# Performance work log

Measured on AMD Instinct MI355X. Metric: run time of the kernel, lower is better.

## Reference

```python
import jax, jax.numpy as jnp
import numpy as np

DIM = 384
HEADS = 6
K = 10          # default k of DynamicGraphAttention
HID = 1536      # int(dim * mlp_ratio)
LN_EPS = 1e-5


def layernorm(x, g, b):
    m = jnp.mean(x, -1, keepdims=True)
    var = jnp.mean((x - m) ** 2, -1, keepdims=True)
    return (x - m) * jax.lax.rsqrt(var + LN_EPS) * g + b


def setup_inputs() -> dict:
    key = jax.random.key(0)
    ks = jax.random.split(key, 12)
    B, N, M, C = 16, 1024, 512, DIM
    s = 0.02
    return dict(
        q=jax.random.normal(ks[0], (B, N, C), jnp.float32),
        v=jax.random.normal(ks[1], (B, M, C), jnp.float32),
        q_pos=jax.random.normal(ks[2], (B, N, 3), jnp.float32),
        v_pos=jax.random.normal(ks[3], (B, M, 3), jnp.float32),
        norm1_g=jnp.ones((C,), jnp.float32), norm1_b=jnp.zeros((C,), jnp.float32),
        qkv_w=jax.random.normal(ks[4], (C, 3 * C), jnp.float32) * s,  # qkv_bias=False
        proj_w=jax.random.normal(ks[5], (C, C), jnp.float32) * s,
        proj_b=jnp.zeros((C,), jnp.float32),
        normq_g=jnp.ones((C,), jnp.float32), normq_b=jnp.zeros((C,), jnp.float32),
        normv_g=jnp.ones((C,), jnp.float32), normv_b=jnp.zeros((C,), jnp.float32),
        knn_w=jax.random.normal(ks[6], (2 * C, C), jnp.float32) * s,
        knn_b=jnp.zeros((C,), jnp.float32),
        norm2_g=jnp.ones((C,), jnp.float32), norm2_b=jnp.zeros((C,), jnp.float32),
        fc1_w=jax.random.normal(ks[7], (C, HID), jnp.float32) * s,
        fc1_b=jnp.zeros((HID,), jnp.float32),
        fc2_w=jax.random.normal(ks[8], (HID, C), jnp.float32) * s,
        fc2_b=jnp.zeros((C,), jnp.float32),
    )


def reference(q, v, q_pos, v_pos,
              norm1_g, norm1_b, qkv_w, proj_w, proj_b,
              normq_g, normq_b, normv_g, normv_b, knn_w, knn_b,
              norm2_g, norm2_b, fc1_w, fc1_b, fc2_w, fc2_b):
    B, N, C = q.shape
    D = C // HEADS

    # --- multi-head self-attention with pre-norm residual ---
    x = layernorm(q, norm1_g, norm1_b)
    qkv = (x @ qkv_w).reshape(B, N, 3, HEADS, D)
    qh, kh, vh = qkv[:, :, 0], qkv[:, :, 1], qkv[:, :, 2]   # [B,N,H,D]
    attn = jnp.einsum('bnhd,bmhd->bhnm', qh, kh) * (D ** -0.5)
    attn = jax.nn.softmax(attn, axis=-1)
    sa = jnp.einsum('bhnm,bmhd->bnhd', attn, vh).reshape(B, N, C)
    sa = sa @ proj_w + proj_b
    q = q + sa

    # --- dynamic graph cross-attention (knn gather + diff-concat MLP + max) ---
    nq = layernorm(q, normq_g, normq_b)          # [B,N,C]
    nv = layernorm(v, normv_g, normv_b)          # [B,M,C]
    # squared distances between query and kv positions: [B,N,M]
    d = (jnp.sum(q_pos ** 2, -1)[:, :, None]
         + jnp.sum(v_pos ** 2, -1)[:, None, :]
         - 2.0 * jnp.einsum('bnc,bmc->bnm', q_pos, v_pos))
    _, idx = jax.lax.top_k(-d, K)                # K nearest neighbors, [B,N,K]
    local_v = jax.vmap(lambda vv, ii: vv[ii])(nv, idx)   # [B,N,K,C]
    qe = nq[:, :, None, :]                                # [B,N,1,C]
    feat = jnp.concatenate(
        [local_v - qe, jnp.broadcast_to(qe, local_v.shape)], axis=-1)  # [B,N,K,2C]
    g = jax.nn.leaky_relu(feat @ knn_w + knn_b, negative_slope=0.2)
    q = q + jnp.max(g, axis=-2)                  # max over K neighbors

    # --- MLP with pre-norm residual ---
    h = layernorm(q, norm2_g, norm2_b)
    h = jax.nn.gelu(h @ fc1_w + fc1_b, approximate=False)
    h = h @ fc2_w + fc2_b
    return q + h
```

## Files before the change

### kernel.cpp

```cpp
#include <hip/hip_runtime.h>
#include <hip/hip_bf16.h>

#define CDIM 384
#define NHEAD 6
#define DHEAD 64
#define BB 16
#define NQ 1024
#define MV 512
#define HIDD 1536
#define KNN 10

typedef __attribute__((ext_vector_type(8))) __bf16 bf16x8;
typedef __attribute__((ext_vector_type(4))) float f32x4;
typedef __attribute__((ext_vector_type(4))) short short4v;

__global__ void cast_all_kernel(const float* __restrict__ qkv_w, const float* __restrict__ proj_w,
                                const float* __restrict__ knn_w, const float* __restrict__ fc1_w,
                                const float* __restrict__ fc2_w,
                                __hip_bfloat16* __restrict__ Wqkv_t,
                                __hip_bfloat16* __restrict__ Wproj_t,
                                __hip_bfloat16* __restrict__ W1_t,
                                __hip_bfloat16* __restrict__ Wd_t,
                                __hip_bfloat16* __restrict__ Wfc1_t,
                                __hip_bfloat16* __restrict__ Wfc2_t) {
  __shared__ float t1[32][33];
  __shared__ float t2[32][33];
  int gid = blockIdx.x;
  int tx = threadIdx.x, ty = threadIdx.y;
  if (gid >= 576 && gid < 720) {
    int id = gid - 576;
    int k0 = (id % 12) * 32, n0 = (id / 12) * 32;
#pragma unroll
    for (int i = 0; i < 4; i++) {
      int k = k0 + ty + i * 8;
      float w1 = knn_w[(size_t)k * CDIM + n0 + tx];
      float w2 = knn_w[(size_t)(CDIM + k) * CDIM + n0 + tx];
      t1[ty + i * 8][tx] = w1;
      t2[ty + i * 8][tx] = w2 - w1;
    }
    __syncthreads();
#pragma unroll
    for (int i = 0; i < 4; i++) {
      W1_t[(size_t)(n0 + ty + i * 8) * CDIM + k0 + tx] = __float2bfloat16(t1[tx][ty + i * 8]);
      Wd_t[(size_t)(n0 + ty + i * 8) * CDIM + k0 + tx] = __float2bfloat16(t2[tx][ty + i * 8]);
    }
    return;
  }
  const float* W;
  __hip_bfloat16* Wt;
  int Kd, Nd, k0, n0;
  if (gid < 432) {
    W = qkv_w; Wt = Wqkv_t; Kd = 384; Nd = 1152;
    k0 = (gid % 12) * 32; n0 = (gid / 12) * 32;
  } else if (gid < 576) {
    int id = gid - 432;
    W = proj_w; Wt = Wproj_t; Kd = 384; Nd = 384;
    k0 = (id % 12) * 32; n0 = (id / 12) * 32;
  } else if (gid < 1296) {
    int id = gid - 720;
    W = fc1_w; Wt = Wfc1_t; Kd = 384; Nd = 1536;
    k0 = (id % 12) * 32; n0 = (id / 12) * 32;
  } else {
    int id = gid - 1296;
    W = fc2_w; Wt = Wfc2_t; Kd = 1536; Nd = 384;
    k0 = (id % 48) * 32; n0 = (id / 48) * 32;
  }
#pragma unroll
  for (int i = 0; i < 4; i++)
    t1[ty + i * 8][tx] = W[(size_t)(k0 + ty + i * 8) * Nd + n0 + tx];
  __syncthreads();
#pragma unroll
  for (int i = 0; i < 4; i++)
    Wt[(size_t)(n0 + ty + i * 8) * Kd + k0 + tx] = __float2bfloat16(t1[tx][ty + i * 8]);
}

__device__ inline void ln_row(const float* __restrict__ xr, const float* __restrict__ gw,
                              const float* __restrict__ bw, __hip_bfloat16* __restrict__ outr,
                              int lane) {
  float v0[6];
  float s = 0.f;
#pragma unroll
  for (int i = 0; i < 3; i++) {
    float2 t = *reinterpret_cast<const float2*>(xr + i * 128 + lane * 2);
    v0[i * 2] = t.x; v0[i * 2 + 1] = t.y; s += t.x + t.y;
  }
  for (int off = 32; off; off >>= 1) s += __shfl_xor(s, off);
  float mean = s * (1.f / 384.f);
  float sq = 0.f;
#pragma unroll
  for (int i = 0; i < 6; i++) { float d = v0[i] - mean; sq += d * d; }
  for (int off = 32; off; off >>= 1) sq += __shfl_xor(sq, off);
  float rstd = rsqrtf(sq * (1.f / 384.f) + 1e-5f);
#pragma unroll
  for (int i = 0; i < 3; i++) {
    int c = i * 128 + lane * 2;
    float2 gg = *reinterpret_cast<const float2*>(gw + c);
    float2 bb = *reinterpret_cast<const float2*>(bw + c);
    __hip_bfloat162 p;
    p.x = __float2bfloat16((v0[i * 2] - mean) * rstd * gg.x + bb.x);
    p.y = __float2bfloat16((v0[i * 2 + 1] - mean) * rstd * gg.y + bb.y);
    *reinterpret_cast<__hip_bfloat162*>(outr + c) = p;
  }
}

__global__ __launch_bounds__(256) void ln_kernel(const float* __restrict__ x,
                                                 const float* __restrict__ gw,
                                                 const float* __restrict__ bw,
                                                 __hip_bfloat16* __restrict__ out, int rows) {
  int wave = (int)((blockIdx.x * blockDim.x + threadIdx.x) >> 6);
  int lane = threadIdx.x & 63;
  if (wave >= rows) return;
  ln_row(x + (size_t)wave * CDIM, gw, bw, out + (size_t)wave * CDIM, lane);
}

__global__ __launch_bounds__(256) void ln_dual_kernel(const float* __restrict__ q1,
                                                      const float* __restrict__ v,
                                                      const float* __restrict__ gq,
                                                      const float* __restrict__ bq,
                                                      const float* __restrict__ gv,
                                                      const float* __restrict__ bv,
                                                      __hip_bfloat16* __restrict__ Xbf,
                                                      __hip_bfloat16* __restrict__ NV) {
  int wave = (int)((blockIdx.x * blockDim.x + threadIdx.x) >> 6);
  int lane = threadIdx.x & 63;
  if (wave < BB * NQ) {
    ln_row(q1 + (size_t)wave * CDIM, gq, bq, Xbf + (size_t)wave * CDIM, lane);
  } else {
    int r = wave - BB * NQ;
    ln_row(v + (size_t)r * CDIM, gv, bv, NV + (size_t)r * CDIM, lane);
  }
}

template <int EPI>
__global__ __launch_bounds__(256) void gemm_kernel(const __hip_bfloat16* __restrict__ A,
                                                   const __hip_bfloat16* __restrict__ Bt,
                                                   const float* __restrict__ bias,
                                                   const float* __restrict__ resid,
                                                   void* __restrict__ outp,
                                                   void* __restrict__ out2,
                                                   void* __restrict__ out3,
                                                   int M, int N, int Kdim) {
  __shared__ __align__(16) __hip_bfloat16 As[128 * 64];
  __shared__ __align__(16) __hip_bfloat16 Bs[128 * 64];
  int m0 = blockIdx.y * 128, n0 = blockIdx.x * 128;
  int t = threadIdx.x;
  int lane = t & 63, w = t >> 6;
  int wrow = w >> 1, wcol = w & 1;
  int lg = lane >> 4, lr = lane & 15;
  int gcol = (((lane & 7) ^ (lane >> 3)) * 8);
  const __hip_bfloat16* Ab = A + (size_t)(m0 + w * 8 + (lane >> 3)) * Kdim + gcol;
  const __hip_bfloat16* Bb = Bt + (size_t)(n0 + w * 8 + (lane >> 3)) * Kdim + gcol;
  char* AsB = (char*)As;
  char* BsB = (char*)Bs;
  f32x4 acc[4][4] = {};
  for (int k0 = 0; k0 < Kdim; k0 += 64) {
    if (k0) __syncthreads();
#pragma unroll
    for (int i = 0; i < 4; i++)
      __builtin_amdgcn_global_load_lds(
          (const __attribute__((address_space(1))) void*)(Ab + (size_t)(i * 32) * Kdim + k0),
          (__attribute__((address_space(3))) void*)(AsB + (i * 4 + w) * 1024), 16, 0, 0);
#pragma unroll
    for (int i = 0; i < 4; i++)
      __builtin_amdgcn_global_load_lds(
          (const __attribute__((address_space(1))) void*)(Bb + (size_t)(i * 32) * Kdim + k0),
          (__attribute__((address_space(3))) void*)(BsB + (i * 4 + w) * 1024), 16, 0, 0);
    __syncthreads();
#pragma unroll
    for (int kk = 0; kk < 2; kk++) {
      bf16x8 a[4], b[4];
#pragma unroll
      for (int i = 0; i < 4; i++) {
        int ra = wrow * 64 + i * 16 + lr;
        int rb = wcol * 64 + i * 16 + lr;
        int sw = (((kk << 2) | lg) ^ (lr & 7)) * 16;
        a[i] = *reinterpret_cast<const bf16x8*>(AsB + ra * 128 + sw);
        b[i] = *reinterpret_cast<const bf16x8*>(BsB + rb * 128 + sw);
      }
#pragma unroll
      for (int i = 0; i < 4; i++)
#pragma unroll
        for (int j = 0; j < 4; j++)
          acc[i][j] = __builtin_amdgcn_mfma_f32_16x16x32_bf16(a[i], b[j], acc[i][j], 0, 0, 0);
    }
  }
#pragma unroll
  for (int i = 0; i < 4; i++)
#pragma unroll
    for (int j = 0; j < 4; j++) {
      int col = n0 + wcol * 64 + j * 16 + lr;
#pragma unroll
      for (int r = 0; r < 4; r++) {
        int row = m0 + wrow * 64 + i * 16 + lg * 4 + r;
        float v = acc[i][j][r];
        if (EPI == 5) {
          int b = row >> 10, n = row & 1023;
          if (col < CDIM) {
            int h = col >> 6, d = col & 63;
            ((__hip_bfloat16*)outp)[(((size_t)(b * NHEAD + h)) * NQ + n) * DHEAD + d] =
                __float2bfloat16(v * 0.18033688f);
          } else if (col < 2 * CDIM) {
            int c = col - CDIM, h = c >> 6, d = c & 63;
            ((__hip_bfloat16*)out2)[(((size_t)(b * NHEAD + h)) * NQ + n) * DHEAD + d] =
                __float2bfloat16(v);
          } else {
            int c = col - 2 * CDIM, h = c >> 6, d = c & 63;
            ((__hip_bfloat16*)out3)[(((size_t)(b * NHEAD + h)) * DHEAD + d) * NQ + n] =
                __float2bfloat16(v);
          }
        } else {
          if (EPI == 1 || EPI == 2 || EPI == 3) v += bias[col];
          if (EPI == 2) v += resid[(size_t)row * N + col];
          if (EPI == 3) v = 0.5f * v * (1.f + erff(v * 0.70710678118654752f));
          if (EPI == 0 || EPI == 3)
            ((__hip_bfloat16*)outp)[(size_t)row * N + col] = __float2bfloat16(v);
          else
            ((float*)outp)[(size_t)row * N + col] = v;
        }
      }
    }
}

__global__ __launch_bounds__(256) void attn_kernel(const __hip_bfloat16* __restrict__ Qb,
                                                   const __hip_bfloat16* __restrict__ Kb,
                                                   const __hip_bfloat16* __restrict__ Vt,
                                                   __hip_bfloat16* __restrict__ SAb) {
  __shared__ __align__(16) __hip_bfloat16 Ks[2][64][72];
  __shared__ __align__(16) __hip_bfloat16 Vs[2][64][72];
  int bh = blockIdx.x % 96;
  int qblk = blockIdx.x / 96;
  int t = threadIdx.x;
  int w = t >> 6, lane = t & 63;
  int lg = lane >> 4, lr = lane & 15;
  const __hip_bfloat16* Qp = Qb + (size_t)bh * NQ * DHEAD;
  const __hip_bfloat16* Kp = Kb + (size_t)bh * NQ * DHEAD;
  const __hip_bfloat16* Vp = Vt + (size_t)bh * DHEAD * NQ;
  int q0 = qblk * 128 + w * 32;
  bf16x8 qf[2][2];
#pragma unroll
  for (int qt = 0; qt < 2; qt++)
#pragma unroll
    for (int kk = 0; kk < 2; kk++)
      qf[qt][kk] = *reinterpret_cast<const bf16x8*>(
          Qp + (size_t)(q0 + qt * 16 + lr) * DHEAD + kk * 32 + lg * 8);
  int srow = w * 16 + (lane >> 2);
  int scol = (lane & 3) * 16;
  uint4 kr0 = *reinterpret_cast<const uint4*>(Kp + (size_t)srow * DHEAD + scol);
  uint4 kr1 = *reinterpret_cast<const uint4*>(Kp + (size_t)srow * DHEAD + scol + 8);
  uint4 vr0 = *reinterpret_cast<const uint4*>(Vp + (size_t)srow * NQ + scol);
  uint4 vr1 = *reinterpret_cast<const uint4*>(Vp + (size_t)srow * NQ + scol + 8);
  *reinterpret_cast<uint4*>(&Ks[0][srow][scol]) = kr0;
  *reinterpret_cast<uint4*>(&Ks[0][srow][scol + 8]) = kr1;
  *reinterpret_cast<uint4*>(&Vs[0][srow][scol]) = vr0;
  *reinterpret_cast<uint4*>(&Vs[0][srow][scol + 8]) = vr1;
  f32x4 o[2][4] = {};
  float m_[2] = {-1e30f, -1e30f};
  float l_[2] = {0.f, 0.f};
  __syncthreads();
  for (int kt = 0; kt < 16; kt++) {
    int cur = kt & 1;
    if (kt < 15) {
      int kb = (kt + 1) * 64;
      kr0 = *reinterpret_cast<const uint4*>(Kp + (size_t)(kb + srow) * DHEAD + scol);
      kr1 = *reinterpret_cast<const uint4*>(Kp + (size_t)(kb + srow) * DHEAD + scol + 8);
      vr0 = *reinterpret_cast<const uint4*>(Vp + (size_t)srow * NQ + kb + scol);
      vr1 = *reinterpret_cast<const uint4*>(Vp + (size_t)srow * NQ + kb + scol + 8);
    }
    f32x4 s[4][2] = {};
#pragma unroll
    for (int kti = 0; kti < 4; kti++)
#pragma unroll
      for (int kk = 0; kk < 2; kk++) {
        bf16x8 a = *reinterpret_cast<const bf16x8*>(&Ks[cur][kti * 16 + lr][kk * 32 + lg * 8]);
#pragma unroll
        for (int qt = 0; qt < 2; qt++)
          s[kti][qt] = __builtin_amdgcn_mfma_f32_16x16x32_bf16(a, qf[qt][kk], s[kti][qt], 0, 0, 0);
      }
#pragma unroll
    for (int qt = 0; qt < 2; qt++) {
      float a0 = fmaxf(fmaxf(s[0][qt][0], s[0][qt][1]), fmaxf(s[0][qt][2], s[0][qt][3]));
      float a1 = fmaxf(fmaxf(s[1][qt][0], s[1][qt][1]), fmaxf(s[1][qt][2], s[1][qt][3]));
      float a2 = fmaxf(fmaxf(s[2][qt][0], s[2][qt][1]), fmaxf(s[2][qt][2], s[2][qt][3]));
      float a3 = fmaxf(fmaxf(s[3][qt][0], s[3][qt][1]), fmaxf(s[3][qt][2], s[3][qt][3]));
      float lmax = fmaxf(fmaxf(a0, a1), fmaxf(a2, a3));
      if (!__all(lmax - m_[qt] <= 8.f)) {
        float pmax = fmaxf(lmax, __shfl_xor(lmax, 16));
        pmax = fmaxf(pmax, __shfl_xor(pmax, 32));
        float mn = fmaxf(m_[qt], pmax);
        float corr = __builtin_amdgcn_exp2f(m_[qt] - mn);
        l_[qt] *= corr;
        m_[qt] = mn;
#pragma unroll
        for (int r = 0; r < 4; r++) {
          float cr = __shfl(corr, (lane & 48) | (((lane >> 4) & 3) * 4 + r));
#pragma unroll
          for (int dt = 0; dt < 4; dt++) o[qt][dt][r] *= cr;
        }
      }
      float m = m_[qt];
      float ls = 0.f;
#pragma unroll
      for (int kti = 0; kti < 4; kti++) {
        float p0 = __builtin_amdgcn_exp2f(s[kti][qt][0] - m);
        float p1 = __builtin_amdgcn_exp2f(s[kti][qt][1] - m);
        float p2 = __builtin_amdgcn_exp2f(s[kti][qt][2] - m);
        float p3 = __builtin_amdgcn_exp2f(s[kti][qt][3] - m);
        s[kti][qt][0] = p0; s[kti][qt][1] = p1; s[kti][qt][2] = p2; s[kti][qt][3] = p3;
        ls += (p0 + p1) + (p2 + p3);
      }
      l_[qt] += ls;
    }
#pragma unroll
    for (int kti = 0; kti < 4; kti++) {
      short4v pa[2];
#pragma unroll
      for (int qt = 0; qt < 2; qt++) {
#pragma unroll
        for (int r = 0; r < 4; r++) {
          __bf16 hv = (__bf16)s[kti][qt][r];
          pa[qt][r] = __builtin_bit_cast(short, hv);
        }
      }
#pragma unroll
      for (int dt = 0; dt < 4; dt++) {
        short4v vb = *reinterpret_cast<const short4v*>(&Vs[cur][dt * 16 + lr][kti * 16 + lg * 4]);
#pragma unroll
        for (int qt = 0; qt < 2; qt++)
          o[qt][dt] = __builtin_amdgcn_mfma_f32_16x16x16bf16_1k(pa[qt], vb, o[qt][dt], 0, 0, 0);
      }
    }
    if (kt < 15) {
      int nb = cur ^ 1;
      *reinterpret_cast<uint4*>(&Ks[nb][srow][scol]) = kr0;
      *reinterpret_cast<uint4*>(&Ks[nb][srow][scol + 8]) = kr1;
      *reinterpret_cast<uint4*>(&Vs[nb][srow][scol]) = vr0;
      *reinterpret_cast<uint4*>(&Vs[nb][srow][scol + 8]) = vr1;
      __syncthreads();
    }
  }
#pragma unroll
  for (int qt = 0; qt < 2; qt++) {
    l_[qt] += __shfl_xor(l_[qt], 16);
    l_[qt] += __shfl_xor(l_[qt], 32);
  }
  int b = bh / NHEAD, h = bh % NHEAD;
#pragma unroll
  for (int qt = 0; qt < 2; qt++)
#pragma unroll
    for (int r = 0; r < 4; r++) {
      float li = __shfl(l_[qt], (lane & 48) | (((lane >> 4) & 3) * 4 + r));
      float inv = 1.f / li;
      int row = q0 + qt * 16 + ((lane >> 4) & 3) * 4 + r;
#pragma unroll
      for (int dt = 0; dt < 4; dt++)
        SAb[((size_t)(b * NQ + row)) * CDIM + h * DHEAD + dt * 16 + lr] =
            __float2bfloat16(o[qt][dt][r] * inv);
    }
}

__global__ __launch_bounds__(256) void knn_fused_kernel(const float* __restrict__ q_pos,
                                                        const float* __restrict__ v_pos,
                                                        const float* __restrict__ A1,
                                                        const float* __restrict__ A2,
                                                        const float* __restrict__ q1,
                                                        const float* __restrict__ g2,
                                                        const float* __restrict__ b2,
                                                        float* __restrict__ q2,
                                                        __hip_bfloat16* __restrict__ xout) {
  int wq = (int)((blockIdx.x * blockDim.x + threadIdx.x) >> 6);
  int lane = threadIdx.x & 63;
  if (wq >= BB * NQ) return;
  int b = wq >> 10;
  const float* qp = q_pos + (size_t)wq * 3;
  double qx = qp[0], qy = qp[1], qz = qp[2];
  double qs = qx * qx + qy * qy + qz * qz;
  double dloc[8];
#pragma unroll
  for (int j = 0; j < 8; j++) {
    int m = lane + 64 * j;
    const float* vp = v_pos + ((size_t)b * MV + m) * 3;
    double vx = vp[0], vy = vp[1], vz = vp[2];
    double vs = vx * vx + vy * vy + vz * vz;
    dloc[j] = qs + vs - 2.0 * (qx * vx + qy * vy + qz * vz);
  }
  float a2[6], mx[6];
#pragma unroll
  for (int i = 0; i < 6; i++) {
    a2[i] = A2[(size_t)wq * CDIM + lane + 64 * i];
    mx[i] = -1e30f;
  }
  for (int k = 0; k < KNN; k++) {
    double best = dloc[0];
    int bj = 0;
#pragma unroll
    for (int j = 1; j < 8; j++)
      if (dloc[j] < best) { best = dloc[j]; bj = j; }
    int bm = lane + 64 * bj;
    for (int off = 1; off < 64; off <<= 1) {
      double od = __shfl_xor(best, off);
      int om = __shfl_xor(bm, off);
      if (od < best || (od == best && om < bm)) { best = od; bm = om; }
    }
    const float* a1 = A1 + ((size_t)b * MV + bm) * CDIM;
#pragma unroll
    for (int i = 0; i < 6; i++) {
      float g = a1[lane + 64 * i] + a2[i];
      g = g > 0.f ? g : 0.2f * g;
      mx[i] = fmaxf(mx[i], g);
    }
#pragma unroll
    for (int j = 0; j < 8; j++)
      if (bm == lane + 64 * j) dloc[j] = 1e300;
  }
  float vals[6];
  float s = 0.f;
#pragma unroll
  for (int i = 0; i < 6; i++) {
    vals[i] = q1[(size_t)wq * CDIM + lane + 64 * i] + mx[i];
    s += vals[i];
  }
  for (int off = 32; off; off >>= 1) s += __shfl_xor(s, off);
  float mean = s * (1.f / 384.f);
  float sq = 0.f;
#pragma unroll
  for (int i = 0; i < 6; i++) { float d = vals[i] - mean; sq += d * d; }
  for (int off = 32; off; off >>= 1) sq += __shfl_xor(sq, off);
  float rstd = rsqrtf(sq * (1.f / 384.f) + 1e-5f);
#pragma unroll
  for (int i = 0; i < 6; i++) {
    int c = lane + 64 * i;
    q2[(size_t)wq * CDIM + c] = vals[i];
    xout[(size_t)wq * CDIM + c] = __float2bfloat16((vals[i] - mean) * rstd * g2[c] + b2[c]);
  }
}

extern "C" void kernel_launch(void* const* d_in, const int* in_sizes, int n_in,
                              void* d_out, int out_size, void* d_ws, size_t ws_size,
                              hipStream_t stream) {
  const float* q = (const float*)d_in[0];
  const float* v = (const float*)d_in[1];
  const float* q_pos = (const float*)d_in[2];
  const float* v_pos = (const float*)d_in[3];
  const float* norm1_g = (const float*)d_in[4];
  const float* norm1_b = (const float*)d_in[5];
  const float* qkv_w = (const float*)d_in[6];
  const float* proj_w = (const float*)d_in[7];
  const float* proj_b = (const float*)d_in[8];
  const float* normq_g = (const float*)d_in[9];
  const float* normq_b = (const float*)d_in[10];
  const float* normv_g = (const float*)d_in[11];
  const float* normv_b = (const float*)d_in[12];
  const float* knn_w = (const float*)d_in[13];
  const float* knn_b = (const float*)d_in[14];
  const float* norm2_g = (const float*)d_in[15];
  const float* norm2_b = (const float*)d_in[16];
  const float* fc1_w = (const float*)d_in[17];
  const float* fc1_b = (const float*)d_in[18];
  const float* fc2_w = (const float*)d_in[19];
  const float* fc2_b = (const float*)d_in[20];

  char* ws = (char*)d_ws;
  const size_t SZ_Wqkv = (size_t)1152 * 384 * 2;
  const size_t SZ_W384 = (size_t)384 * 384 * 2;
  const size_t SZ_Wfc = (size_t)1536 * 384 * 2;
  const size_t SZ_Xbf = (size_t)16384 * 384 * 2;
  const size_t SZ_QKV = (size_t)16384 * 1152 * 2;
  const size_t SZ_q32 = (size_t)16384 * 384 * 4;
  const size_t SZ_NV = (size_t)8192 * 384 * 2;

  size_t o_Wqkv = 0;
  size_t o_Wproj = o_Wqkv + SZ_Wqkv;
  size_t o_W1 = o_Wproj + SZ_W384;
  size_t o_Wd = o_W1 + SZ_W384;
  size_t o_Wfc1 = o_Wd + SZ_W384;
  size_t o_Wfc2 = o_Wfc1 + SZ_Wfc;
  size_t o_Xbf = o_Wfc2 + SZ_Wfc;
  size_t o_QKV = o_Xbf + SZ_Xbf;
  size_t o_A1 = o_QKV;
  size_t o_A2 = o_QKV + (size_t)8192 * 384 * 4;
  size_t o_Qb = o_QKV + SZ_QKV;
  size_t o_Kb = o_Qb + SZ_Xbf;
  size_t o_Vt = o_Kb + SZ_Xbf;
  size_t o_SA = o_Vt + SZ_Xbf;
  size_t o_H1 = o_Qb;
  size_t o_q1 = o_SA + SZ_Xbf;
  size_t o_NV = o_q1 + SZ_q32;
  size_t o_q2 = o_NV + SZ_NV;

  __hip_bfloat16* Wqkv_t = (__hip_bfloat16*)(ws + o_Wqkv);
  __hip_bfloat16* Wproj_t = (__hip_bfloat16*)(ws + o_Wproj);
  __hip_bfloat16* W1_t = (__hip_bfloat16*)(ws + o_W1);
  __hip_bfloat16* Wd_t = (__hip_bfloat16*)(ws + o_Wd);
  __hip_bfloat16* Wfc1_t = (__hip_bfloat16*)(ws + o_Wfc1);
  __hip_bfloat16* Wfc2_t = (__hip_bfloat16*)(ws + o_Wfc2);
  __hip_bfloat16* Xbf = (__hip_bfloat16*)(ws + o_Xbf);
  float* A1f = (float*)(ws + o_A1);
  float* A2f = (float*)(ws + o_A2);
  __hip_bfloat16* Qb = (__hip_bfloat16*)(ws + o_Qb);
  __hip_bfloat16* Kb = (__hip_bfloat16*)(ws + o_Kb);
  __hip_bfloat16* Vt = (__hip_bfloat16*)(ws + o_Vt);
  __hip_bfloat16* SAb = (__hip_bfloat16*)(ws + o_SA);
  __hip_bfloat16* H1 = (__hip_bfloat16*)(ws + o_H1);
  float* q1 = (float*)(ws + o_q1);
  __hip_bfloat16* NV = (__hip_bfloat16*)(ws + o_NV);
  float* q2 = (float*)(ws + o_q2);
  float* outf = (float*)d_out;

  cast_all_kernel<<<1872, dim3(32, 8), 0, stream>>>(qkv_w, proj_w, knn_w, fc1_w, fc2_w,
                                                    Wqkv_t, Wproj_t, W1_t, Wd_t, Wfc1_t, Wfc2_t);
  ln_kernel<<<4096, 256, 0, stream>>>(q, norm1_g, norm1_b, Xbf, 16384);
  gemm_kernel<5><<<dim3(9, 128), 256, 0, stream>>>(Xbf, Wqkv_t, nullptr, nullptr,
                                                   Qb, Kb, Vt, 16384, 1152, 384);
  attn_kernel<<<768, 256, 0, stream>>>(Qb, Kb, Vt, SAb);
  gemm_kernel<2><<<dim3(3, 128), 256, 0, stream>>>(SAb, Wproj_t, proj_b, q, q1,
                                                   nullptr, nullptr, 16384, 384, 384);
  ln_dual_kernel<<<6144, 256, 0, stream>>>(q1, v, normq_g, normq_b, normv_g, normv_b, Xbf, NV);
  gemm_kernel<4><<<dim3(3, 64), 256, 0, stream>>>(NV, W1_t, nullptr, nullptr, A1f,
                                                  nullptr, nullptr, 8192, 384, 384);
  gemm_kernel<1><<<dim3(3, 128), 256, 0, stream>>>(Xbf, Wd_t, knn_b, nullptr, A2f,
                                                   nullptr, nullptr, 16384, 384, 384);
  knn_fused_kernel<<<4096, 256, 0, stream>>>(q_pos, v_pos, A1f, A2f, q1,
                                             norm2_g, norm2_b, q2, Xbf);
  gemm_kernel<3><<<dim3(12, 128), 256, 0, stream>>>(Xbf, Wfc1_t, fc1_b, nullptr, H1,
                                                    nullptr, nullptr, 16384, 1536, 384);
  gemm_kernel<2><<<dim3(3, 128), 256, 0, stream>>>(H1, Wfc2_t, fc2_b, q2, outf,
                                                   nullptr, nullptr, 16384, 384, 1536);
}
```

Baseline: 335.1 us.

## Merge prep kernels, fuse knn GEMMs, shrink attention tiles for occupancy

Merges the weight cast/transpose kernel with the first layernorm into one prep launch, and folds the two knn-branch GEMMs (NV·W1 and Xbf·Wd) into a single launch that picks operands by block row. The attention kernel is reworked to give each wave 16 queries instead of 32 and to use 32-key tiles, with launch bounds asking for 6 blocks per CU, doubling the grid. The goal is fewer launches and higher occupancy in attention. The cost is less reuse of each K/V tile and twice as many synchronisation steps per block. The merged GEMM relies on W1_t and Wd_t sitting next to each other in the workspace.

```diff
diff --git a/kernel.cpp b/kernel.cpp
--- a/kernel.cpp
+++ b/kernel.cpp
@@ -14,19 +14,54 @@
 typedef __attribute__((ext_vector_type(4))) float f32x4;
 typedef __attribute__((ext_vector_type(4))) short short4v;
 
-__global__ void cast_all_kernel(const float* __restrict__ qkv_w, const float* __restrict__ proj_w,
-                                const float* __restrict__ knn_w, const float* __restrict__ fc1_w,
-                                const float* __restrict__ fc2_w,
-                                __hip_bfloat16* __restrict__ Wqkv_t,
-                                __hip_bfloat16* __restrict__ Wproj_t,
-                                __hip_bfloat16* __restrict__ W1_t,
-                                __hip_bfloat16* __restrict__ Wd_t,
-                                __hip_bfloat16* __restrict__ Wfc1_t,
-                                __hip_bfloat16* __restrict__ Wfc2_t) {
+__device__ inline void ln_row(const float* __restrict__ xr, const float* __restrict__ gw,
+                              const float* __restrict__ bw, __hip_bfloat16* __restrict__ outr,
+                              int lane) {
+  float v0[6];
+  float s = 0.f;
+#pragma unroll
+  for (int i = 0; i < 3; i++) {
+    float2 t = *reinterpret_cast<const float2*>(xr + i * 128 + lane * 2);
+    v0[i * 2] = t.x; v0[i * 2 + 1] = t.y; s += t.x + t.y;
+  }
+  for (int off = 32; off; off >>= 1) s += __shfl_xor(s, off);
+  float mean = s * (1.f / 384.f);
+  float sq = 0.f;
+#pragma unroll
+  for (int i = 0; i < 6; i++) { float d = v0[i] - mean; sq += d * d; }
+  for (int off = 32; off; off >>= 1) sq += __shfl_xor(sq, off);
+  float rstd = rsqrtf(sq * (1.f / 384.f) + 1e-5f);
+#pragma unroll
+  for (int i = 0; i < 3; i++) {
+    int c = i * 128 + lane * 2;
+    float2 gg = *reinterpret_cast<const float2*>(gw + c);
+    float2 bb = *reinterpret_cast<const float2*>(bw + c);
+    __hip_bfloat162 p;
+    p.x = __float2bfloat16((v0[i * 2] - mean) * rstd * gg.x + bb.x);
+    p.y = __float2bfloat16((v0[i * 2 + 1] - mean) * rstd * gg.y + bb.y);
+    *reinterpret_cast<__hip_bfloat162*>(outr + c) = p;
+  }
+}
+
+__global__ __launch_bounds__(256) void prep_kernel(
+    const float* __restrict__ qkv_w, const float* __restrict__ proj_w,
+    const float* __restrict__ knn_w, const float* __restrict__ fc1_w,
+    const float* __restrict__ fc2_w, const float* __restrict__ q,
+    const float* __restrict__ g1, const float* __restrict__ b1,
+    __hip_bfloat16* __restrict__ Wqkv_t, __hip_bfloat16* __restrict__ Wproj_t,
+    __hip_bfloat16* __restrict__ W1_t, __hip_bfloat16* __restrict__ Wd_t,
+    __hip_bfloat16* __restrict__ Wfc1_t, __hip_bfloat16* __restrict__ Wfc2_t,
+    __hip_bfloat16* __restrict__ Xbf) {
+  int gid = blockIdx.x;
+  if (gid >= 1872) {
+    int wave = (gid - 1872) * 4 + ((int)threadIdx.x >> 6);
+    int lane = threadIdx.x & 63;
+    ln_row(q + (size_t)wave * CDIM, g1, b1, Xbf + (size_t)wave * CDIM, lane);
+    return;
+  }
   __shared__ float t1[32][33];
   __shared__ float t2[32][33];
-  int gid = blockIdx.x;
-  int tx = threadIdx.x, ty = threadIdx.y;
+  int tx = threadIdx.x & 31, ty = (int)threadIdx.x >> 5;
   if (gid >= 576 && gid < 720) {
     int id = gid - 576;
     int k0 = (id % 12) * 32, n0 = (id / 12) * 32;
@@ -74,45 +109,6 @@
     Wt[(size_t)(n0 + ty + i * 8) * Kd + k0 + tx] = __float2bfloat16(t1[tx][ty + i * 8]);
 }
 
-__device__ inline void ln_row(const float* __restrict__ xr, const float* __restrict__ gw,
-                              const float* __restrict__ bw, __hip_bfloat16* __restrict__ outr,
-                              int lane) {
-  float v0[6];
-  float s = 0.f;
-#pragma unroll
-  for (int i = 0; i < 3; i++) {
-    float2 t = *reinterpret_cast<const float2*>(xr + i * 128 + lane * 2);
-    v0[i * 2] = t.x; v0[i * 2 + 1] = t.y; s += t.x + t.y;
-  }
-  for (int off = 32; off; off >>= 1) s += __shfl_xor(s, off);
-  float mean = s * (1.f / 384.f);
-  float sq = 0.f;
-#pragma unroll
-  for (int i = 0; i < 6; i++) { float d = v0[i] - mean; sq += d * d; }
-  for (int off = 32; off; off >>= 1) sq += __shfl_xor(sq, off);
-  float rstd = rsqrtf(sq * (1.f / 384.f) + 1e-5f);
-#pragma unroll
-  for (int i = 0; i < 3; i++) {
-    int c = i * 128 + lane * 2;
-    float2 gg = *reinterpret_cast<const float2*>(gw + c);
-    float2 bb = *reinterpret_cast<const float2*>(bw + c);
-    __hip_bfloat162 p;
-    p.x = __float2bfloat16((v0[i * 2] - mean) * rstd * gg.x + bb.x);
-    p.y = __float2bfloat16((v0[i * 2 + 1] - mean) * rstd * gg.y + bb.y);
-    *reinterpret_cast<__hip_bfloat162*>(outr + c) = p;
-  }
-}
-
-__global__ __launch_bounds__(256) void ln_kernel(const float* __restrict__ x,
-                                                 const float* __restrict__ gw,
-                                                 const float* __restrict__ bw,
-                                                 __hip_bfloat16* __restrict__ out, int rows) {
-  int wave = (int)((blockIdx.x * blockDim.x + threadIdx.x) >> 6);
-  int lane = threadIdx.x & 63;
-  if (wave >= rows) return;
-  ln_row(x + (size_t)wave * CDIM, gw, bw, out + (size_t)wave * CDIM, lane);
-}
-
 __global__ __launch_bounds__(256) void ln_dual_kernel(const float* __restrict__ q1,
                                                       const float* __restrict__ v,
                                                       const float* __restrict__ gq,
@@ -143,13 +139,25 @@
   __shared__ __align__(16) __hip_bfloat16 As[128 * 64];
   __shared__ __align__(16) __hip_bfloat16 Bs[128 * 64];
   int m0 = blockIdx.y * 128, n0 = blockIdx.x * 128;
+  const __hip_bfloat16* Ause = A;
+  const __hip_bfloat16* Bt_use = Bt;
+  bool isA1 = false;
+  if (EPI == 6) {
+    if (blockIdx.y >= 128) {
+      isA1 = true;
+      m0 = (blockIdx.y - 128) * 128;
+      Ause = (const __hip_bfloat16*)out3;
+    } else {
+      Bt_use = Bt + (size_t)384 * 384;
+    }
+  }
   int t = threadIdx.x;
   int lane = t & 63, w = t >> 6;
   int wrow = w >> 1, wcol = w & 1;
   int lg = lane >> 4, lr = lane & 15;
   int gcol = (((lane & 7) ^ (lane >> 3)) * 8);
-  const __hip_bfloat16* Ab = A + (size_t)(m0 + w * 8 + (lane >> 3)) * Kdim + gcol;
-  const __hip_bfloat16* Bb = Bt + (size_t)(n0 + w * 8 + (lane >> 3)) * Kdim + gcol;
+  const __hip_bfloat16* Ab = Ause + (size_t)(m0 + w * 8 + (lane >> 3)) * Kdim + gcol;
+  const __hip_bfloat16* Bb = Bt_use + (size_t)(n0 + w * 8 + (lane >> 3)) * Kdim + gcol;
   char* AsB = (char*)As;
   char* BsB = (char*)Bs;
   f32x4 acc[4][4] = {};
@@ -208,6 +216,11 @@
             ((__hip_bfloat16*)out3)[(((size_t)(b * NHEAD + h)) * DHEAD + d) * NQ + n] =
                 __float2bfloat16(v);
           }
+        } else if (EPI == 6) {
+          float vv = v;
+          if (!isA1) vv += bias[col];
+          float* dst = isA1 ? (float*)out2 : (float*)outp;
+          dst[(size_t)row * 384 + col] = vv;
         } else {
           if (EPI == 1 || EPI == 2 || EPI == 3) v += bias[col];
           if (EPI == 2) v += resid[(size_t)row * N + col];
@@ -221,12 +234,12 @@
     }
 }
 
-__global__ __launch_bounds__(256) void attn_kernel(const __hip_bfloat16* __restrict__ Qb,
-                                                   const __hip_bfloat16* __restrict__ Kb,
-                                                   const __hip_bfloat16* __restrict__ Vt,
-                                                   __hip_bfloat16* __restrict__ SAb) {
-  __shared__ __align__(16) __hip_bfloat16 Ks[2][64][72];
-  __shared__ __align__(16) __hip_bfloat16 Vs[2][64][72];
+__global__ __launch_bounds__(256, 6) void attn_kernel(const __hip_bfloat16* __restrict__ Qb,
+                                                      const __hip_bfloat16* __restrict__ Kb,
+                                                      const __hip_bfloat16* __restrict__ Vt,
+                                                      __hip_bfloat16* __restrict__ SAb) {
+  __shared__ __align__(16) __hip_bfloat16 Ks[2][32][72];
+  __shared__ __align__(16) __hip_bfloat16 Vs[2][64][40];
   int bh = blockIdx.x % 96;
   int qblk = blockIdx.x / 96;
   int t = threadIdx.x;
@@ -235,127 +248,98 @@
   const __hip_bfloat16* Qp = Qb + (size_t)bh * NQ * DHEAD;
   const __hip_bfloat16* Kp = Kb + (size_t)bh * NQ * DHEAD;
   const __hip_bfloat16* Vp = Vt + (size_t)bh * DHEAD * NQ;
-  int q0 = qblk * 128 + w * 32;
-  bf16x8 qf[2][2];
-#pragma unroll
-  for (int qt = 0; qt < 2; qt++)
-#pragma unroll
-    for (int kk = 0; kk < 2; kk++)
-      qf[qt][kk] = *reinterpret_cast<const bf16x8*>(
-          Qp + (size_t)(q0 + qt * 16 + lr) * DHEAD + kk * 32 + lg * 8);
-  int srow = w * 16 + (lane >> 2);
-  int scol = (lane & 3) * 16;
-  uint4 kr0 = *reinterpret_cast<const uint4*>(Kp + (size_t)srow * DHEAD + scol);
-  uint4 kr1 = *reinterpret_cast<const uint4*>(Kp + (size_t)srow * DHEAD + scol + 8);
-  uint4 vr0 = *reinterpret_cast<const uint4*>(Vp + (size_t)srow * NQ + scol);
-  uint4 vr1 = *reinterpret_cast<const uint4*>(Vp + (size_t)srow * NQ + scol + 8);
-  *reinterpret_cast<uint4*>(&Ks[0][srow][scol]) = kr0;
-  *reinterpret_cast<uint4*>(&Ks[0][srow][scol + 8]) = kr1;
-  *reinterpret_cast<uint4*>(&Vs[0][srow][scol]) = vr0;
-  *reinterpret_cast<uint4*>(&Vs[0][srow][scol + 8]) = vr1;
-  f32x4 o[2][4] = {};
-  float m_[2] = {-1e30f, -1e30f};
-  float l_[2] = {0.f, 0.f};
+  int q0 = qblk * 64 + w * 16;
+  bf16x8 qf[2];
+#pragma unroll
+  for (int kk = 0; kk < 2; kk++)
+    qf[kk] = *reinterpret_cast<const bf16x8*>(
+        Qp + (size_t)(q0 + lr) * DHEAD + kk * 32 + lg * 8);
+  int krow = t >> 3, kcol = (t & 7) * 8;
+  int vrow = t >> 2, vcol = (t & 3) * 8;
+  uint4 kr = *reinterpret_cast<const uint4*>(Kp + (size_t)krow * DHEAD + kcol);
+  uint4 vr = *reinterpret_cast<const uint4*>(Vp + (size_t)vrow * NQ + vcol);
+  *reinterpret_cast<uint4*>(&Ks[0][krow][kcol]) = kr;
+  *reinterpret_cast<uint4*>(&Vs[0][vrow][vcol]) = vr;
+  f32x4 o[4] = {};
+  float m_ = -1e30f, l_ = 0.f;
   __syncthreads();
-  for (int kt = 0; kt < 16; kt++) {
+  for (int kt = 0; kt < 32; kt++) {
     int cur = kt & 1;
-    if (kt < 15) {
-      int kb = (kt + 1) * 64;
-      kr0 = *reinterpret_cast<const uint4*>(Kp + (size_t)(kb + srow) * DHEAD + scol);
-      kr1 = *reinterpret_cast<const uint4*>(Kp + (size_t)(kb + srow) * DHEAD + scol + 8);
-      vr0 = *reinterpret_cast<const uint4*>(Vp + (size_t)srow * NQ + kb + scol);
-      vr1 = *reinterpret_cast<const uint4*>(Vp + (size_t)srow * NQ + kb + scol + 8);
-    }
-    f32x4 s[4][2] = {};
-#pragma unroll
-    for (int kti = 0; kti < 4; kti++)
+    if (kt < 31) {
+      int kb = (kt + 1) * 32;
+      kr = *reinterpret_cast<const uint4*>(Kp + (size_t)(kb + krow) * DHEAD + kcol);
+      vr = *reinterpret_cast<const uint4*>(Vp + (size_t)vrow * NQ + kb + vcol);
+    }
+    f32x4 s[2] = {};
+#pragma unroll
+    for (int kti = 0; kti < 2; kti++)
 #pragma unroll
       for (int kk = 0; kk < 2; kk++) {
         bf16x8 a = *reinterpret_cast<const bf16x8*>(&Ks[cur][kti * 16 + lr][kk * 32 + lg * 8]);
-#pragma unroll
-        for (int qt = 0; qt < 2; qt++)
-          s[kti][qt] = __builtin_amdgcn_mfma_f32_16x16x32_bf16(a, qf[qt][kk], s[kti][qt], 0, 0, 0);
-      }
-#pragma unroll
-    for (int qt = 0; qt < 2; qt++) {
-      float a0 = fmaxf(fmaxf(s[0][qt][0], s[0][qt][1]), fmaxf(s[0][qt][2], s[0][qt][3]));
-      float a1 = fmaxf(fmaxf(s[1][qt][0], s[1][qt][1]), fmaxf(s[1][qt][2], s[1][qt][3]));
-      float a2 = fmaxf(fmaxf(s[2][qt][0], s[2][qt][1]), fmaxf(s[2][qt][2], s[2][qt][3]));
-      float a3 = fmaxf(fmaxf(s[3][qt][0], s[3][qt][1]), fmaxf(s[3][qt][2], s[3][qt][3]));
-      float lmax = fmaxf(fmaxf(a0, a1), fmaxf(a2, a3));
-      if (!__all(lmax - m_[qt] <= 8.f)) {
+        s[kti] = __builtin_amdgcn_mfma_f32_16x16x32_bf16(a, qf[kk], s[kti], 0, 0, 0);
+      }
+    {
+      float a0 = fmaxf(fmaxf(s[0][0], s[0][1]), fmaxf(s[0][2], s[0][3]));
+      float a1 = fmaxf(fmaxf(s[1][0], s[1][1]), fmaxf(s[1][2], s[1][3]));
+      float lmax = fmaxf(a0, a1);
+      if (!__all(lmax - m_ <= 8.f)) {
         float pmax = fmaxf(lmax, __shfl_xor(lmax, 16));
         pmax = fmaxf(pmax, __shfl_xor(pmax, 32));
-        float mn = fmaxf(m_[qt], pmax);
-        float corr = __builtin_amdgcn_exp2f(m_[qt] - mn);
-        l_[qt] *= corr;
-        m_[qt] = mn;
+        float mn = fmaxf(m_, pmax);
+        float corr = __builtin_amdgcn_exp2f(m_ - mn);
+        l_ *= corr;
+        m_ = mn;
 #pragma unroll
         for (int r = 0; r < 4; r++) {
-          float cr = __shfl(corr, (lane & 48) | (((lane >> 4) & 3) * 4 + r));
-#pragma unroll
-          for (int dt = 0; dt < 4; dt++) o[qt][dt][r] *= cr;
+          float cr = __shfl(corr, (lane & 48) | (lg * 4 + r));
+#pragma unroll
+          for (int dt = 0; dt < 4; dt++) o[dt][r] *= cr;
         }
       }
-      float m = m_[qt];
-      float ls = 0.f;
-#pragma unroll
-      for (int kti = 0; kti < 4; kti++) {
-        float p0 = __builtin_amdgcn_exp2f(s[kti][qt][0] - m);
-        float p1 = __builtin_amdgcn_exp2f(s[kti][qt][1] - m);
-        float p2 = __builtin_amdgcn_exp2f(s[kti][qt][2] - m);
-        float p3 = __builtin_amdgcn_exp2f(s[kti][qt][3] - m);
-        s[kti][qt][0] = p0; s[kti][qt][1] = p1; s[kti][qt][2] = p2; s[kti][qt][3] = p3;
-        ls += (p0 + p1) + (p2 + p3);
-      }
-      l_[qt] += ls;
-    }
-#pragma unroll
-    for (int kti = 0; kti < 4; kti++) {
-      short4v pa[2];
-#pragma unroll
-      for (int qt = 0; qt < 2; qt++) {
-#pragma unroll
-        for (int r = 0; r < 4; r++) {
-          __bf16 hv = (__bf16)s[kti][qt][r];
-          pa[qt][r] = __builtin_bit_cast(short, hv);
-        }
+#pragma unroll
+      for (int kti = 0; kti < 2; kti++) {
+        float p0 = __builtin_amdgcn_exp2f(s[kti][0] - m_);
+        float p1 = __builtin_amdgcn_exp2f(s[kti][1] - m_);
+        float p2 = __builtin_amdgcn_exp2f(s[kti][2] - m_);
+        float p3 = __builtin_amdgcn_exp2f(s[kti][3] - m_);
+        s[kti][0] = p0; s[kti][1] = p1; s[kti][2] = p2; s[kti][3] = p3;
+        l_ += (p0 + p1) + (p2 + p3);
+      }
+    }
+#pragma unroll
+    for (int kti = 0; kti < 2; kti++) {
+      short4v pa;
+#pragma unroll
+      for (int r = 0; r < 4; r++) {
+        __bf16 hv = (__bf16)s[kti][r];
+        pa[r] = __builtin_bit_cast(short, hv);
       }
 #pragma unroll
       for (int dt = 0; dt < 4; dt++) {
         short4v vb = *reinterpret_cast<const short4v*>(&Vs[cur][dt * 16 + lr][kti * 16 + lg * 4]);
-#pragma unroll
-        for (int qt = 0; qt < 2; qt++)
-          o[qt][dt] = __builtin_amdgcn_mfma_f32_16x16x16bf16_1k(pa[qt], vb, o[qt][dt], 0, 0, 0);
-      }
-    }
-    if (kt < 15) {
+        o[dt] = __builtin_amdgcn_mfma_f32_16x16x16bf16_1k(pa, vb, o[dt], 0, 0, 0);
+      }
+    }
+    if (kt < 31) {
       int nb = cur ^ 1;
-      *reinterpret_cast<uint4*>(&Ks[nb][srow][scol]) = kr0;
-      *reinterpret_cast<uint4*>(&Ks[nb][srow][scol + 8]) = kr1;
-      *reinterpret_cast<uint4*>(&Vs[nb][srow][scol]) = vr0;
-      *reinterpret_cast<uint4*>(&Vs[nb][srow][scol + 8]) = vr1;
+      *reinterpret_cast<uint4*>(&Ks[nb][krow][kcol]) = kr;
+      *reinterpret_cast<uint4*>(&Vs[nb][vrow][vcol]) = vr;
       __syncthreads();
     }
   }
-#pragma unroll
-  for (int qt = 0; qt < 2; qt++) {
-    l_[qt] += __shfl_xor(l_[qt], 16);
-    l_[qt] += __shfl_xor(l_[qt], 32);
-  }
+  l_ += __shfl_xor(l_, 16);
+  l_ += __shfl_xor(l_, 32);
   int b = bh / NHEAD, h = bh % NHEAD;
 #pragma unroll
-  for (int qt = 0; qt < 2; qt++)
-#pragma unroll
-    for (int r = 0; r < 4; r++) {
-      float li = __shfl(l_[qt], (lane & 48) | (((lane >> 4) & 3) * 4 + r));
-      float inv = 1.f / li;
-      int row = q0 + qt * 16 + ((lane >> 4) & 3) * 4 + r;
-#pragma unroll
-      for (int dt = 0; dt < 4; dt++)
-        SAb[((size_t)(b * NQ + row)) * CDIM + h * DHEAD + dt * 16 + lr] =
-            __float2bfloat16(o[qt][dt][r] * inv);
-    }
+  for (int r = 0; r < 4; r++) {
+    float li = __shfl(l_, (lane & 48) | (lg * 4 + r));
+    float inv = 1.f / li;
+    int row = q0 + lg * 4 + r;
+#pragma unroll
+    for (int dt = 0; dt < 4; dt++)
+      SAb[((size_t)(b * NQ + row)) * CDIM + h * DHEAD + dt * 16 + lr] =
+          __float2bfloat16(o[dt][r] * inv);
+  }
 }
 
 __global__ __launch_bounds__(256) void knn_fused_kernel(const float* __restrict__ q_pos,
@@ -506,19 +490,17 @@
   float* q2 = (float*)(ws + o_q2);
   float* outf = (float*)d_out;
 
-  cast_all_kernel<<<1872, dim3(32, 8), 0, stream>>>(qkv_w, proj_w, knn_w, fc1_w, fc2_w,
-                                                    Wqkv_t, Wproj_t, W1_t, Wd_t, Wfc1_t, Wfc2_t);
-  ln_kernel<<<4096, 256, 0, stream>>>(q, norm1_g, norm1_b, Xbf, 16384);
+  prep_kernel<<<5968, 256, 0, stream>>>(qkv_w, proj_w, knn_w, fc1_w, fc2_w, q,
+                                        norm1_g, norm1_b,
+                                        Wqkv_t, Wproj_t, W1_t, Wd_t, Wfc1_t, Wfc2_t, Xbf);
   gemm_kernel<5><<<dim3(9, 128), 256, 0, stream>>>(Xbf, Wqkv_t, nullptr, nullptr,
                                                    Qb, Kb, Vt, 16384, 1152, 384);
-  attn_kernel<<<768, 256, 0, stream>>>(Qb, Kb, Vt, SAb);
+  attn_kernel<<<1536, 256, 0, stream>>>(Qb, Kb, Vt, SAb);
   gemm_kernel<2><<<dim3(3, 128), 256, 0, stream>>>(SAb, Wproj_t, proj_b, q, q1,
                                                    nullptr, nullptr, 16384, 384, 384);
   ln_dual_kernel<<<6144, 256, 0, stream>>>(q1, v, normq_g, normq_b, normv_g, normv_b, Xbf, NV);
-  gemm_kernel<4><<<dim3(3, 64), 256, 0, stream>>>(NV, W1_t, nullptr, nullptr, A1f,
-                                                  nullptr, nullptr, 8192, 384, 384);
-  gemm_kernel<1><<<dim3(3, 128), 256, 0, stream>>>(Xbf, Wd_t, knn_b, nullptr, A2f,
-                                                   nullptr, nullptr, 16384, 384, 384);
+  gemm_kernel<6><<<dim3(3, 192), 256, 0, stream>>>(Xbf, W1_t, knn_b, nullptr, A2f,
+                                                   A1f, (void*)NV, 16384, 384, 384);
   knn_fused_kernel<<<4096, 256, 0, stream>>>(q_pos, v_pos, A1f, A2f, q1,
                                              norm2_g, norm2_b, q2, Xbf);
   gemm_kernel<3><<<dim3(12, 128), 256, 0, stream>>>(Xbf, Wfc1_t, fc1_b, nullptr, H1,
```

Result: no change. 330.6 us (-1.3%).
